# Kernel tuning notes

Measured on AMD Instinct MI355X. Metric: run time of the kernel, lower is better.

The kernel has to match this reference:

```python
import jax, jax.numpy as jnp
import numpy as np

B, T, H, A = 64, 512, 1024, 256  # T == max_sen_len by construction of attention_u
PAD_VAL = -2.0 ** 22


def setup_inputs() -> dict:
    key = jax.random.key(0)
    k1, k2, k3, k4 = jax.random.split(key, 4)
    inputs = jax.random.normal(k1, (B, T, H), dtype=jnp.float32)
    sen_len = jax.random.randint(k2, (B,), 1, T + 1, dtype=jnp.int32)
    W = jax.random.normal(k3, (H, A), dtype=jnp.float32) * (1.0 / np.sqrt(H))
    b = jnp.zeros((A,), dtype=jnp.float32)
    U = jax.random.normal(k4, (A, T), dtype=jnp.float32) * (1.0 / np.sqrt(A))
    return {"inputs": inputs, "sen_len": sen_len, "W": W, "b": b, "U": U}


def reference(inputs, sen_len, W, b, U):
    # Dense with tanh: [B,T,H] @ [H,A] -> [B,T,A]
    alpha = jnp.tanh(jnp.einsum('bth,ha->bta', inputs, W) + b)
    # Score against attention_u: [B,T,A] @ [A,T] -> [B,T,T]
    scores = jnp.einsum('bta,as->bts', alpha, U)
    # sequence mask over last (key) dim, broadcast over query dim
    mask = jnp.arange(T)[None, :] < sen_len[:, None]        # [B,T]
    scores = jnp.where(mask[:, None, :], scores, jnp.float32(PAD_VAL))
    p = jax.nn.softmax(scores, axis=-1)                     # [B,T,T]
    # Weighted sum pooling: [B,T,T] @ [B,T,H] -> [B,T,H]
    Z = jnp.einsum('bts,bsh->bth', p, inputs)
    # dropout: is_training=False -> identity
    return Z
```

## Files before the change

kernel.cpp:

```cpp
#include <hip/hip_runtime.h>
#include <hip/hip_bf16.h>

typedef short short8 __attribute__((ext_vector_type(8)));
typedef short short4v __attribute__((ext_vector_type(4)));
typedef float f32x4 __attribute__((ext_vector_type(4)));
typedef __bf16 bf16x8 __attribute__((ext_vector_type(8)));

template <int ROWS>
__device__ __forceinline__ void stage2(const __hip_bfloat16* __restrict__ g,
                                       int ld, short* lds, int t) {
    const int w = t >> 6;
    const int lane = t & 63;
#pragma unroll
    for (int i = 0; i < ROWS / 64; ++i) {
        const int cb = i * 512 + w * 64;
        const int c = cb + lane;
        const int row = c >> 3;
        const int kc = (c & 7) ^ (row & 7);
        __builtin_amdgcn_global_load_lds((const void*)(g + (long)row * ld + kc * 8),
                                         (void*)(lds + cb * 8), 16, 0, 0);
    }
}

__global__ __launch_bounds__(512, 2) void gemm_xw_kernel(
    const float* __restrict__ Xf,
    const __hip_bfloat16* __restrict__ Wt,
    __hip_bfloat16* __restrict__ alpha,
    const float* __restrict__ bias) {
    __shared__ __align__(16) short sm[2][24576];

    int bx = blockIdx.x, by = blockIdx.y;
    {
        const int nx = gridDim.x, ny = gridDim.y;
        const int nwg = nx * ny;
        const int lin = bx + nx * by;
        const int swz = (lin & 7) * (nwg >> 3) + (lin >> 3);
        bx = swz % nx;
        by = swz / nx;
    }

    const int t = threadIdx.x;
    const int w = t >> 6, lane = t & 63;
    const int wm = w >> 1, wn = w & 1;
    const int fr = lane & 15, quad = lane >> 4;

    const float* Ab = Xf + (long)by * 256 * 1024;
    const __hip_bfloat16* Bb = Wt + (long)bx * 128 * 1024;

    int arow[4], akc[4];
#pragma unroll
    for (int i = 0; i < 4; ++i) {
        const int c = i * 512 + t;
        arow[i] = c >> 3;
        akc[i] = ((c & 7) ^ (arow[i] & 7)) * 8;
    }

    f32x4 acc[4][4] = {};
    float4 rA[4][2];

#pragma unroll
    for (int i = 0; i < 4; ++i) {
        const float* src = Ab + (long)arow[i] * 1024 + akc[i];
        rA[i][0] = *(const float4*)(src);
        rA[i][1] = *(const float4*)(src + 4);
    }
    stage2<128>(Bb, 1024, &sm[0][16384], t);
#pragma unroll
    for (int i = 0; i < 4; ++i) {
        const int c = i * 512 + t;
        __hip_bfloat16 tmp[8] __attribute__((aligned(16)));
        tmp[0] = __float2bfloat16(rA[i][0].x); tmp[1] = __float2bfloat16(rA[i][0].y);
        tmp[2] = __float2bfloat16(rA[i][0].z); tmp[3] = __float2bfloat16(rA[i][0].w);
        tmp[4] = __float2bfloat16(rA[i][1].x); tmp[5] = __float2bfloat16(rA[i][1].y);
        tmp[6] = __float2bfloat16(rA[i][1].z); tmp[7] = __float2bfloat16(rA[i][1].w);
        *(short8*)(void*)&sm[0][c * 8] = *(short8*)(void*)tmp;
    }
    __syncthreads();

    int cur = 0;
    for (int kt = 0; kt < 16; ++kt) {
        const bool more = kt + 1 < 16;
        if (more) {
#pragma unroll
            for (int i = 0; i < 4; ++i) {
                const float* src = Ab + (long)arow[i] * 1024 + (kt + 1) * 64 + akc[i];
                rA[i][0] = *(const float4*)(src);
                rA[i][1] = *(const float4*)(src + 4);
            }
            stage2<128>(Bb + (kt + 1) * 64, 1024, &sm[cur ^ 1][16384], t);
        }
        const short* At = &sm[cur][0];
        const short* Bts = &sm[cur][16384];
#pragma unroll
        for (int ks = 0; ks < 2; ++ks) {
            bf16x8 af[4], bfv[4];
            const int kc = ks * 4 + quad;
#pragma unroll
            for (int m = 0; m < 4; ++m) {
                const int row = wm * 64 + m * 16 + fr;
                const int chunk = row * 8 + (kc ^ (row & 7));
                af[m] = *(const bf16x8*)(const void*)(At + chunk * 8);
            }
#pragma unroll
            for (int n = 0; n < 4; ++n) {
                const int row = wn * 64 + n * 16 + fr;
                const int chunk = row * 8 + (kc ^ (row & 7));
                bfv[n] = *(const bf16x8*)(const void*)(Bts + chunk * 8);
            }
#pragma unroll
            for (int m = 0; m < 4; ++m)
#pragma unroll
                for (int n = 0; n < 4; ++n)
                    acc[m][n] = __builtin_amdgcn_mfma_f32_16x16x32_bf16(
                        af[m], bfv[n], acc[m][n], 0, 0, 0);
        }
        if (more) {
#pragma unroll
            for (int i = 0; i < 4; ++i) {
                const int c = i * 512 + t;
                __hip_bfloat16 tmp[8] __attribute__((aligned(16)));
                tmp[0] = __float2bfloat16(rA[i][0].x); tmp[1] = __float2bfloat16(rA[i][0].y);
                tmp[2] = __float2bfloat16(rA[i][0].z); tmp[3] = __float2bfloat16(rA[i][0].w);
                tmp[4] = __float2bfloat16(rA[i][1].x); tmp[5] = __float2bfloat16(rA[i][1].y);
                tmp[6] = __float2bfloat16(rA[i][1].z); tmp[7] = __float2bfloat16(rA[i][1].w);
                *(short8*)(void*)&sm[cur ^ 1][c * 8] = *(short8*)(void*)tmp;
            }
            __syncthreads();
        }
        cur ^= 1;
    }

    const long rowBase = (long)by * 256 + wm * 64;
    const int colBase = bx * 128 + wn * 64;
#pragma unroll
    for (int m = 0; m < 4; ++m) {
#pragma unroll
        for (int n = 0; n < 4; ++n) {
            const int col = colBase + n * 16 + fr;
            const float bv = bias[col];
#pragma unroll
            for (int j = 0; j < 4; ++j) {
                const long row = rowBase + m * 16 + quad * 4 + j;
                alpha[row * 256 + col] = __float2bfloat16(tanhf(acc[m][n][j] + bv));
            }
        }
    }
}

__global__ __launch_bounds__(512, 4) void gemm_pv_kernel(
    const __hip_bfloat16* __restrict__ P,
    const float* __restrict__ Xf,
    float* __restrict__ Z) {
    __shared__ __align__(16) short smA[3][8192];
    __shared__ __align__(16) short smB[2][5120];

    int bx = blockIdx.x, by = blockIdx.y, bz = blockIdx.z;
    {
        const int nx = gridDim.x, ny = gridDim.y;
        const int nwg = nx * ny * gridDim.z;
        const int lin = bx + nx * (by + ny * bz);
        const int swz = (lin & 7) * (nwg >> 3) + (lin >> 3);
        bx = swz % nx;
        const int r = swz / nx;
        by = r % ny;
        bz = r / ny;
    }

    const int t = threadIdx.x;
    const int w = t >> 6, lane = t & 63;
    const int wm = w >> 1, wn = w & 1;
    const int fr = lane & 15, quad = lane >> 4;

    const __hip_bfloat16* Ab = P + ((long)bz * 512 + by * 256) * 512;
    const float* Bb = Xf + (long)bz * 512 * 1024 + bx * 128;

    int acb[2], arow[2], akc[2];
#pragma unroll
    for (int i = 0; i < 2; ++i) {
        acb[i] = i * 512 + w * 64;
        const int s = acb[i] + lane;
        arow[i] = s >> 2;
        akc[i] = ((s & 3) ^ ((arow[i] >> 1) & 3)) * 8;
    }
    const int bi = t & 15;
    const int bhc = t >> 4;

    f32x4 acc[4][4] = {};
    float4 r0, r1;

#define PV_ISSUE_A(KT, BUF)                                                     \
    _Pragma("unroll") for (int i = 0; i < 2; ++i)                               \
        __builtin_amdgcn_global_load_lds(                                       \
            (const void*)(Ab + (long)arow[i] * 512 + (KT) * 32 + akc[i]),       \
            (void*)(&smA[BUF][acb[i] * 8]), 16, 0, 0);

#define PV_LOAD_B(KT)                                                           \
    {                                                                           \
        const float* s0 = Bb + (long)((KT) * 32 + 2 * bi) * 1024 + bhc * 4;     \
        r0 = *(const float4*)(s0);                                              \
        r1 = *(const float4*)(s0 + 1024);                                       \
    }

#define PV_WRITE_B(BUF)                                                         \
    {                                                                           \
        int* dst = (int*)(void*)&smB[BUF][(bhc * 4) * 40 + bi * 2];             \
        _Pragma("unroll") for (int j = 0; j < 4; ++j) {                         \
            __hip_bfloat16 h0 = __float2bfloat16(((const float*)&r0)[j]);       \
            __hip_bfloat16 h1 = __float2bfloat16(((const float*)&r1)[j]);       \
            dst[j * 20] = (int)*(unsigned short*)&h0 |                          \
                          ((int)*(unsigned short*)&h1 << 16);                   \
        }                                                                       \
    }

    PV_ISSUE_A(0, 0)
    PV_ISSUE_A(1, 1)
    PV_LOAD_B(0)
    PV_WRITE_B(0)
    PV_LOAD_B(1)
    __builtin_amdgcn_sched_barrier(0);
    asm volatile("s_waitcnt vmcnt(4)" ::: "memory");
    asm volatile("s_waitcnt lgkmcnt(0)" ::: "memory");
    __builtin_amdgcn_s_barrier();
    __builtin_amdgcn_sched_barrier(0);

#pragma unroll
    for (int k = 0; k < 16; ++k) {
        if (k + 2 < 16) PV_ISSUE_A(k + 2, (k + 2) % 3)
        {
            const short* At = &smA[k % 3][0];
            const short* Bt = &smB[k % 2][0];
            bf16x8 bfv[4];
#pragma unroll
            for (int n = 0; n < 4; ++n) {
                const int h = wn * 64 + n * 16 + fr;
                bfv[n] = *(const bf16x8*)(const void*)(Bt + h * 40 + quad * 8);
            }
#pragma unroll
            for (int m = 0; m < 4; ++m) {
                const int row = wm * 64 + m * 16 + fr;
                const int slot = row * 4 + (quad ^ ((row >> 1) & 3));
                const bf16x8 af = *(const bf16x8*)(const void*)(At + slot * 8);
#pragma unroll
                for (int n = 0; n < 4; ++n)
                    acc[m][n] = __builtin_amdgcn_mfma_f32_16x16x32_bf16(
                        af, bfv[n], acc[m][n], 0, 0, 0);
            }
        }
        if (k + 1 < 16) PV_WRITE_B((k + 1) % 2)
        if (k + 2 < 16) PV_LOAD_B(k + 2)
        __builtin_amdgcn_sched_barrier(0);
        if (k + 2 < 16) {
            asm volatile("s_waitcnt vmcnt(4)" ::: "memory");
        } else if (k + 1 < 16) {
            asm volatile("s_waitcnt vmcnt(0)" ::: "memory");
        }
        if (k + 1 < 16) {
            asm volatile("s_waitcnt lgkmcnt(0)" ::: "memory");
            __builtin_amdgcn_s_barrier();
            __builtin_amdgcn_sched_barrier(0);
        }
    }
#undef PV_ISSUE_A
#undef PV_LOAD_B
#undef PV_WRITE_B

    const long rowBase = (long)bz * 512 + by * 256 + wm * 64;
    const int colBase = bx * 128 + wn * 64;
#pragma unroll
    for (int m = 0; m < 4; ++m) {
#pragma unroll
        for (int n = 0; n < 4; ++n) {
            const int col = colBase + n * 16 + fr;
#pragma unroll
            for (int j = 0; j < 4; ++j) {
                const long row = rowBase + m * 16 + quad * 4 + j;
                Z[row * 1024 + col] = acc[m][n][j];
            }
        }
    }
}

__global__ __launch_bounds__(256) void transpose_cvt_kernel(const float* __restrict__ in,
                                                            __hip_bfloat16* __restrict__ out,
                                                            int R, int C) {
    const int o = blockIdx.x * 256 + threadIdx.x;
    if (o >= R * C) return;
    const int c = o / R;
    const int r = o - c * R;
    out[o] = __float2bfloat16(in[(long)r * C + c]);
}

__global__ __launch_bounds__(512) void score_softmax_kernel(
    const __hip_bfloat16* __restrict__ Aa,
    const __hip_bfloat16* __restrict__ Ut,
    __hip_bfloat16* __restrict__ P,
    const int* __restrict__ sen) {
    __shared__ __align__(16) short At[64 * 64];
    __shared__ __align__(16) short Bts[512 * 64];
    __shared__ float red[2][64][9];

    const int t = threadIdx.x;
    const int w = t >> 6, lane = t & 63;
    const int fr = lane & 15, quad = lane >> 4;
    const long row0 = (long)blockIdx.x * 64;
    const __hip_bfloat16* Ab = Aa + row0 * 256;

    f32x4 acc[4][4] = {};

    for (int kt = 0; kt < 4; ++kt) {
        if (kt) __syncthreads();
        {
            const int cb = w * 64;
            const int c = cb + lane;
            const int row = c >> 3, kc = (c & 7) ^ (row & 7);
            __builtin_amdgcn_global_load_lds(
                (const void*)(Ab + (long)row * 256 + kt * 64 + kc * 8),
                (void*)(At + cb * 8), 16, 0, 0);
        }
#pragma unroll
        for (int i = 0; i < 8; ++i) {
            const int cb = i * 512 + w * 64;
            const int c = cb + lane;
            const int row = c >> 3, kc = (c & 7) ^ (row & 7);
            __builtin_amdgcn_global_load_lds(
                (const void*)(Ut + (long)row * 256 + kt * 64 + kc * 8),
                (void*)(Bts + cb * 8), 16, 0, 0);
        }
        __syncthreads();
#pragma unroll
        for (int ks = 0; ks < 2; ++ks) {
            bf16x8 af[4], bfv[4];
            const int kc = ks * 4 + quad;
#pragma unroll
            for (int m = 0; m < 4; ++m) {
                const int row = m * 16 + fr;
                const int chunk = row * 8 + (kc ^ (row & 7));
                af[m] = *(const bf16x8*)(const void*)(At + chunk * 8);
            }
#pragma unroll
            for (int n = 0; n < 4; ++n) {
                const int row = w * 64 + n * 16 + fr;
                const int chunk = row * 8 + (kc ^ (row & 7));
                bfv[n] = *(const bf16x8*)(const void*)(Bts + chunk * 8);
            }
#pragma unroll
            for (int m = 0; m < 4; ++m)
#pragma unroll
                for (int n = 0; n < 4; ++n)
                    acc[m][n] = __builtin_amdgcn_mfma_f32_16x16x32_bf16(
                        af[m], bfv[n], acc[m][n], 0, 0, 0);
        }
    }
    __syncthreads();

    const int L = sen[row0 >> 9];
    bool valid[4];
#pragma unroll
    for (int n = 0; n < 4; ++n) valid[n] = (w * 64 + n * 16 + fr) < L;

    float mx[4][4];
#pragma unroll
    for (int m = 0; m < 4; ++m)
#pragma unroll
        for (int j = 0; j < 4; ++j) {
            float v = -3.0e38f;
#pragma unroll
            for (int n = 0; n < 4; ++n)
                if (valid[n]) v = fmaxf(v, acc[m][n][j]);
#pragma unroll
            for (int off = 8; off >= 1; off >>= 1) v = fmaxf(v, __shfl_xor(v, off, 64));
            mx[m][j] = v;
        }
    if (fr == 0) {
#pragma unroll
        for (int m = 0; m < 4; ++m)
#pragma unroll
            for (int j = 0; j < 4; ++j) red[0][m * 16 + quad * 4 + j][w] = mx[m][j];
    }
    __syncthreads();
    float rmax[4][4];
#pragma unroll
    for (int m = 0; m < 4; ++m)
#pragma unroll
        for (int j = 0; j < 4; ++j) {
            const int row = m * 16 + quad * 4 + j;
            float v = red[0][row][0];
#pragma unroll
            for (int ww = 1; ww < 8; ++ww) v = fmaxf(v, red[0][row][ww]);
            rmax[m][j] = v;
        }

    float sum[4][4];
#pragma unroll
    for (int m = 0; m < 4; ++m)
#pragma unroll
        for (int j = 0; j < 4; ++j) {
            float s = 0.f;
#pragma unroll
            for (int n = 0; n < 4; ++n) {
                float e = valid[n] ? __expf(acc[m][n][j] - rmax[m][j]) : 0.f;
                acc[m][n][j] = e;
                s += e;
            }
#pragma unroll
            for (int off = 8; off >= 1; off >>= 1) s += __shfl_xor(s, off, 64);
            sum[m][j] = s;
        }
    if (fr == 0) {
#pragma unroll
        for (int m = 0; m < 4; ++m)
#pragma unroll
            for (int j = 0; j < 4; ++j) red[1][m * 16 + quad * 4 + j][w] = sum[m][j];
    }
    __syncthreads();
#pragma unroll
    for (int m = 0; m < 4; ++m)
#pragma unroll
        for (int j = 0; j < 4; ++j) {
            const int row = m * 16 + quad * 4 + j;
            float s = 0.f;
#pragma unroll
            for (int ww = 0; ww < 8; ++ww) s += red[1][row][ww];
            const float inv = 1.f / s;
#pragma unroll
            for (int n = 0; n < 4; ++n)
                P[(row0 + row) * 512 + w * 64 + n * 16 + fr] =
                    __float2bfloat16(acc[m][n][j] * inv);
        }
}

extern "C" void kernel_launch(void* const* d_in, const int* in_sizes, int n_in,
                              void* d_out, int out_size, void* d_ws, size_t ws_size,
                              hipStream_t stream) {
    const float* X = (const float*)d_in[0];
    const int* sen = (const int*)d_in[1];
    const float* W = (const float*)d_in[2];
    const float* bias = (const float*)d_in[3];
    const float* U = (const float*)d_in[4];
    float* out = (float*)d_out;

    const int B = 64, T = 512, H = 1024, A = 256;
    const long M = (long)B * T;

    char* ws = (char*)d_ws;
    __hip_bfloat16* Pbf = (__hip_bfloat16*)ws;
    __hip_bfloat16* Wt = (__hip_bfloat16*)(ws + M * T * 2);
    __hip_bfloat16* Ut = (__hip_bfloat16*)((char*)Wt + (long)H * A * 2);

    __hip_bfloat16* alpha = (__hip_bfloat16*)((char*)d_out + M * H * 2);

    transpose_cvt_kernel<<<(H * A) / 256, 256, 0, stream>>>(W, Wt, H, A);
    transpose_cvt_kernel<<<(A * T) / 256, 256, 0, stream>>>(U, Ut, A, T);
    gemm_xw_kernel<<<dim3(2, 128), 512, 0, stream>>>(X, Wt, alpha, bias);
    score_softmax_kernel<<<(int)(M / 64), 512, 0, stream>>>(alpha, Ut, Pbf, sen);
    gemm_pv_kernel<<<dim3(H / 128, T / 256, B), 512, 0, stream>>>(Pbf, X, out);
}
```

Baseline: 144.1 us.

## Halve XW GEMM M-tile and add triple-buffered B pipeline with explicit waitcnts

The X·W GEMM tile shrinks from 256 to 128 rows, doubling the grid to 512 workgroups and raising launch bounds to 4 blocks per CU. The W operand moves to a three-stage LDS ring filled by async global_load_lds, while X is prefetched two iterations ahead through registers. Barriers use explicit vmcnt/lgkmcnt waits and sched_barriers. The aim is better occupancy and more latency hiding for the fp32 X loads, at the cost of re-reading W tiles more often and fragile hand-tuned wait counts.

```diff
diff --git a/kernel.cpp b/kernel.cpp
--- a/kernel.cpp
+++ b/kernel.cpp
@@ -22,12 +22,13 @@
     }
 }
 
-__global__ __launch_bounds__(512, 2) void gemm_xw_kernel(
+__global__ __launch_bounds__(512, 4) void gemm_xw_kernel(
     const float* __restrict__ Xf,
     const __hip_bfloat16* __restrict__ Wt,
     __hip_bfloat16* __restrict__ alpha,
     const float* __restrict__ bias) {
-    __shared__ __align__(16) short sm[2][24576];
+    __shared__ __align__(16) short smB[3][8192];
+    __shared__ __align__(16) short smA[2][8192];
 
     int bx = blockIdx.x, by = blockIdx.y;
     {
@@ -44,96 +45,106 @@
     const int wm = w >> 1, wn = w & 1;
     const int fr = lane & 15, quad = lane >> 4;
 
-    const float* Ab = Xf + (long)by * 256 * 1024;
+    const float* Ab = Xf + (long)by * 128 * 1024;
     const __hip_bfloat16* Bb = Wt + (long)bx * 128 * 1024;
 
-    int arow[4], akc[4];
-#pragma unroll
-    for (int i = 0; i < 4; ++i) {
-        const int c = i * 512 + t;
-        arow[i] = c >> 3;
-        akc[i] = ((c & 7) ^ (arow[i] & 7)) * 8;
-    }
-
-    f32x4 acc[4][4] = {};
-    float4 rA[4][2];
-
-#pragma unroll
-    for (int i = 0; i < 4; ++i) {
-        const float* src = Ab + (long)arow[i] * 1024 + akc[i];
-        rA[i][0] = *(const float4*)(src);
-        rA[i][1] = *(const float4*)(src + 4);
-    }
-    stage2<128>(Bb, 1024, &sm[0][16384], t);
-#pragma unroll
-    for (int i = 0; i < 4; ++i) {
-        const int c = i * 512 + t;
-        __hip_bfloat16 tmp[8] __attribute__((aligned(16)));
-        tmp[0] = __float2bfloat16(rA[i][0].x); tmp[1] = __float2bfloat16(rA[i][0].y);
-        tmp[2] = __float2bfloat16(rA[i][0].z); tmp[3] = __float2bfloat16(rA[i][0].w);
-        tmp[4] = __float2bfloat16(rA[i][1].x); tmp[5] = __float2bfloat16(rA[i][1].y);
-        tmp[6] = __float2bfloat16(rA[i][1].z); tmp[7] = __float2bfloat16(rA[i][1].w);
-        *(short8*)(void*)&sm[0][c * 8] = *(short8*)(void*)tmp;
-    }
-    __syncthreads();
-
-    int cur = 0;
-    for (int kt = 0; kt < 16; ++kt) {
-        const bool more = kt + 1 < 16;
-        if (more) {
-#pragma unroll
-            for (int i = 0; i < 4; ++i) {
-                const float* src = Ab + (long)arow[i] * 1024 + (kt + 1) * 64 + akc[i];
-                rA[i][0] = *(const float4*)(src);
-                rA[i][1] = *(const float4*)(src + 4);
-            }
-            stage2<128>(Bb + (kt + 1) * 64, 1024, &sm[cur ^ 1][16384], t);
-        }
-        const short* At = &sm[cur][0];
-        const short* Bts = &sm[cur][16384];
-#pragma unroll
-        for (int ks = 0; ks < 2; ++ks) {
-            bf16x8 af[4], bfv[4];
-            const int kc = ks * 4 + quad;
-#pragma unroll
-            for (int m = 0; m < 4; ++m) {
-                const int row = wm * 64 + m * 16 + fr;
-                const int chunk = row * 8 + (kc ^ (row & 7));
-                af[m] = *(const bf16x8*)(const void*)(At + chunk * 8);
-            }
-#pragma unroll
-            for (int n = 0; n < 4; ++n) {
-                const int row = wn * 64 + n * 16 + fr;
-                const int chunk = row * 8 + (kc ^ (row & 7));
-                bfv[n] = *(const bf16x8*)(const void*)(Bts + chunk * 8);
-            }
-#pragma unroll
-            for (int m = 0; m < 4; ++m)
-#pragma unroll
-                for (int n = 0; n < 4; ++n)
-                    acc[m][n] = __builtin_amdgcn_mfma_f32_16x16x32_bf16(
-                        af[m], bfv[n], acc[m][n], 0, 0, 0);
-        }
-        if (more) {
-#pragma unroll
-            for (int i = 0; i < 4; ++i) {
-                const int c = i * 512 + t;
-                __hip_bfloat16 tmp[8] __attribute__((aligned(16)));
-                tmp[0] = __float2bfloat16(rA[i][0].x); tmp[1] = __float2bfloat16(rA[i][0].y);
-                tmp[2] = __float2bfloat16(rA[i][0].z); tmp[3] = __float2bfloat16(rA[i][0].w);
-                tmp[4] = __float2bfloat16(rA[i][1].x); tmp[5] = __float2bfloat16(rA[i][1].y);
-                tmp[6] = __float2bfloat16(rA[i][1].z); tmp[7] = __float2bfloat16(rA[i][1].w);
-                *(short8*)(void*)&sm[cur ^ 1][c * 8] = *(short8*)(void*)tmp;
-            }
-            __syncthreads();
-        }
-        cur ^= 1;
-    }
-
-    const long rowBase = (long)by * 256 + wm * 64;
+    int acs[2], arow[2], akc[2];
+#pragma unroll
+    for (int i = 0; i < 2; ++i) {
+        acs[i] = i * 512 + t;
+        arow[i] = acs[i] >> 3;
+        akc[i] = ((acs[i] & 7) ^ (arow[i] & 7)) * 8;
+    }
+
+    f32x4 acc[2][4] = {};
+    float4 rA[2][2];
+
+#define XW_ISSUE_B(KT, BUF) stage2<128>(Bb + (KT) * 64, 1024, &smB[BUF][0], t);
+
+#define XW_LOAD_A(KT)                                                           \
+    _Pragma("unroll") for (int i = 0; i < 2; ++i) {                             \
+        const float* src = Ab + (long)arow[i] * 1024 + (KT) * 64 + akc[i];      \
+        rA[i][0] = *(const float4*)(src);                                       \
+        rA[i][1] = *(const float4*)(src + 4);                                   \
+    }
+
+#define XW_WRITE_A(BUF)                                                         \
+    _Pragma("unroll") for (int i = 0; i < 2; ++i) {                             \
+        __hip_bfloat16 tmp[8] __attribute__((aligned(16)));                     \
+        tmp[0] = __float2bfloat16(rA[i][0].x);                                  \
+        tmp[1] = __float2bfloat16(rA[i][0].y);                                  \
+        tmp[2] = __float2bfloat16(rA[i][0].z);                                  \
+        tmp[3] = __float2bfloat16(rA[i][0].w);                                  \
+        tmp[4] = __float2bfloat16(rA[i][1].x);                                  \
+        tmp[5] = __float2bfloat16(rA[i][1].y);                                  \
+        tmp[6] = __float2bfloat16(rA[i][1].z);                                  \
+        tmp[7] = __float2bfloat16(rA[i][1].w);                                  \
+        *(short8*)(void*)&smA[BUF][acs[i] * 8] = *(short8*)(void*)tmp;          \
+    }
+
+    XW_ISSUE_B(0, 0)
+    XW_ISSUE_B(1, 1)
+    XW_LOAD_A(0)
+    XW_WRITE_A(0)
+    XW_LOAD_A(1)
+    __builtin_amdgcn_sched_barrier(0);
+    asm volatile("s_waitcnt vmcnt(4)" ::: "memory");
+    asm volatile("s_waitcnt lgkmcnt(0)" ::: "memory");
+    __builtin_amdgcn_s_barrier();
+    __builtin_amdgcn_sched_barrier(0);
+
+#pragma unroll
+    for (int k = 0; k < 16; ++k) {
+        if (k + 2 < 16) XW_ISSUE_B(k + 2, (k + 2) % 3)
+        {
+            const short* At = &smA[k % 2][0];
+            const short* Bt = &smB[k % 3][0];
+#pragma unroll
+            for (int ks = 0; ks < 2; ++ks) {
+                bf16x8 af[2], bfv[4];
+                const int kc = ks * 4 + quad;
+#pragma unroll
+                for (int m = 0; m < 2; ++m) {
+                    const int row = wm * 32 + m * 16 + fr;
+                    const int chunk = row * 8 + (kc ^ (row & 7));
+                    af[m] = *(const bf16x8*)(const void*)(At + chunk * 8);
+                }
+#pragma unroll
+                for (int n = 0; n < 4; ++n) {
+                    const int row = wn * 64 + n * 16 + fr;
+                    const int chunk = row * 8 + (kc ^ (row & 7));
+                    bfv[n] = *(const bf16x8*)(const void*)(Bt + chunk * 8);
+                }
+#pragma unroll
+                for (int m = 0; m < 2; ++m)
+#pragma unroll
+                    for (int n = 0; n < 4; ++n)
+                        acc[m][n] = __builtin_amdgcn_mfma_f32_16x16x32_bf16(
+                            af[m], bfv[n], acc[m][n], 0, 0, 0);
+            }
+        }
+        if (k + 1 < 16) XW_WRITE_A((k + 1) % 2)
+        if (k + 2 < 16) XW_LOAD_A(k + 2)
+        __builtin_amdgcn_sched_barrier(0);
+        if (k + 2 < 16) {
+            asm volatile("s_waitcnt vmcnt(6)" ::: "memory");
+        } else if (k + 1 < 16) {
+            asm volatile("s_waitcnt vmcnt(0)" ::: "memory");
+        }
+        if (k + 1 < 16) {
+            asm volatile("s_waitcnt lgkmcnt(0)" ::: "memory");
+            __builtin_amdgcn_s_barrier();
+            __builtin_amdgcn_sched_barrier(0);
+        }
+    }
+#undef XW_ISSUE_B
+#undef XW_LOAD_A
+#undef XW_WRITE_A
+
+    const long rowBase = (long)by * 128 + wm * 32;
     const int colBase = bx * 128 + wn * 64;
 #pragma unroll
-    for (int m = 0; m < 4; ++m) {
+    for (int m = 0; m < 2; ++m) {
 #pragma unroll
         for (int n = 0; n < 4; ++n) {
             const int col = colBase + n * 16 + fr;
@@ -451,7 +462,7 @@
 
     transpose_cvt_kernel<<<(H * A) / 256, 256, 0, stream>>>(W, Wt, H, A);
     transpose_cvt_kernel<<<(A * T) / 256, 256, 0, stream>>>(U, Ut, A, T);
-    gemm_xw_kernel<<<dim3(2, 128), 512, 0, stream>>>(X, Wt, alpha, bias);
+    gemm_xw_kernel<<<dim3(2, 256), 512, 0, stream>>>(X, Wt, alpha, bias);
     score_softmax_kernel<<<(int)(M / 64), 512, 0, stream>>>(alpha, Ut, Pbf, sen);
     gemm_pv_kernel<<<dim3(H / 128, T / 256, B), 512, 0, stream>>>(Pbf, X, out);
 }
```

New measurement: 139.4 us. 1.03x faster.
